# Kernel optimization log

Measured on AMD Instinct MI355X. Metric: run time of the kernel, lower is better.

The kernel has to match this reference:

```python
import jax, jax.numpy as jnp
import numpy as np
from jax import lax

T, B = 256, 64
VOCAB, EMB, HID, NLAB = 100000, 300, 256, 20
PAD_WORD = 0


def setup_inputs() -> dict:
    key = jax.random.key(0)
    ks = jax.random.split(key, 16)
    sentences = jax.random.randint(ks[0], (T, B), 0, VOCAB)
    sentences = sentences.at[0].set(jnp.maximum(sentences[0], 1))  # mask[0] must be all on (torchcrf)
    labels = jax.random.randint(ks[1], (T, B), 0, NLAB)
    s = 0.05
    emb = jax.random.normal(ks[2], (VOCAB, EMB), jnp.float32) * s
    Wih_f = jax.random.normal(ks[3], (4 * HID, EMB), jnp.float32) * s
    Whh_f = jax.random.normal(ks[4], (4 * HID, HID), jnp.float32) * s
    b_f = jax.random.normal(ks[5], (4 * HID,), jnp.float32) * s
    Wih_b = jax.random.normal(ks[6], (4 * HID, EMB), jnp.float32) * s
    Whh_b = jax.random.normal(ks[7], (4 * HID, HID), jnp.float32) * s
    b_b = jax.random.normal(ks[8], (4 * HID,), jnp.float32) * s
    W_top = jax.random.normal(ks[9], (NLAB, 2 * HID), jnp.float32) * s
    b_top = jax.random.normal(ks[10], (NLAB,), jnp.float32) * s
    start_t = jax.random.normal(ks[11], (NLAB,), jnp.float32) * 0.1
    end_t = jax.random.normal(ks[12], (NLAB,), jnp.float32) * 0.1
    trans = jax.random.normal(ks[13], (NLAB, NLAB), jnp.float32) * 0.1
    return dict(emb=emb, Wih_f=Wih_f, Whh_f=Whh_f, b_f=b_f, Wih_b=Wih_b,
                Whh_b=Whh_b, b_b=b_b, W_top=W_top, b_top=b_top,
                start_t=start_t, end_t=end_t, trans=trans,
                sentences=sentences, labels=labels)


def _lstm_dir(x, W_ih, W_hh, b, reverse):
    # x: (T, B, E) -> hs: (T, B, H); torch gate order i,f,g,o
    H = W_hh.shape[1]
    x_proj = jnp.einsum('tbe,ge->tbg', x, W_ih) + b  # precompute input projection

    def step(carry, xp):
        h, c = carry
        gates = xp + h @ W_hh.T
        i, f, g, o = jnp.split(gates, 4, axis=-1)
        c = jax.nn.sigmoid(f) * c + jax.nn.sigmoid(i) * jnp.tanh(g)
        h = jax.nn.sigmoid(o) * jnp.tanh(c)
        return (h, c), h

    init = (jnp.zeros((x.shape[1], H), x.dtype), jnp.zeros((x.shape[1], H), x.dtype))
    _, hs = lax.scan(step, init, x_proj, reverse=reverse)
    return hs


def _crf_nll(emissions, tags, mask, start_t, end_t, trans):
    # emissions: (T,B,L), tags: (T,B), mask: (T,B) bool. torchcrf math, reduction='sum'.
    Tn, Bn, L = emissions.shape
    maskf = mask.astype(emissions.dtype)
    barange = jnp.arange(Bn)
    # numerator
    score = start_t[tags[0]] + emissions[0, barange, tags[0]]
    trans_sc = trans[tags[:-1], tags[1:]]  # (T-1, B)
    emit_sc = jnp.take_along_axis(emissions[1:], tags[1:, :, None], axis=2)[..., 0]
    score = score + ((trans_sc + emit_sc) * maskf[1:]).sum(0)
    seq_ends = mask.astype(jnp.int32).sum(0) - 1  # (B,)
    last_tags = jnp.take_along_axis(tags, seq_ends[None, :], axis=0)[0]
    score = score + end_t[last_tags]
    # partition (log-sum-exp forward recurrence)
    alpha0 = start_t[None, :] + emissions[0]  # (B, L)

    def step(alpha, inp):
        emis_t, m_t = inp
        nxt = jax.nn.logsumexp(alpha[:, :, None] + trans[None] + emis_t[:, None, :], axis=1)
        return jnp.where(m_t[:, None], nxt, alpha), None

    alpha, _ = lax.scan(step, alpha0, (emissions[1:], mask[1:]))
    denom = jax.nn.logsumexp(alpha + end_t[None, :], axis=1)
    llh = (score - denom).sum()
    return -llh


def reference(emb, Wih_f, Whh_f, b_f, Wih_b, Whh_b, b_b, W_top, b_top,
              start_t, end_t, trans, sentences, labels):
    x = emb[sentences]  # (T, B, E)
    h_f = _lstm_dir(x, Wih_f, Whh_f, b_f, reverse=False)
    h_b = _lstm_dir(x, Wih_b, Whh_b, b_b, reverse=True)
    rnn_out = jnp.concatenate([h_f, h_b], axis=-1)  # (T, B, 2H)
    emissions = jnp.einsum('tbh,lh->tbl', rnn_out, W_top) + b_top
    mask = sentences != PAD_WORD
    return _crf_nll(emissions, labels, mask, start_t, end_t, trans)
```

## Files before the change

### kernel.cpp

```cpp
#include <hip/hip_runtime.h>
#include <hip/hip_bf16.h>

#define T_    256
#define B_    64
#define EMB_  300
#define HID_  256
#define G_    1024
#define L_    20
#define M_    (T_*B_)

#define NCL   32
#define CLB   8
#define BPC   4
#define UPB   32

typedef float f32x4 __attribute__((ext_vector_type(4)));
typedef unsigned long long u64;

__global__ __launch_bounds__(256) void k_xproj(
    const float* __restrict__ emb,
    const float* __restrict__ Wih_f, const float* __restrict__ b_f,
    const float* __restrict__ Wih_b, const float* __restrict__ b_b,
    const int*   __restrict__ sent,
    float* __restrict__ xp)
{
    __shared__ float As[16][68];
    __shared__ float Bs[16][68];
    __shared__ int   words[64];

    const int tid = threadIdx.x;
    const int n0  = blockIdx.x * 64;
    const int m0  = blockIdx.y * 64;
    const int dir = n0 >> 10;
    const int g0  = n0 & 1023;
    const float* __restrict__ Wih  = dir ? Wih_b : Wih_f;
    const float* __restrict__ bias = dir ? b_b   : b_f;

    if (tid < 64) words[tid] = sent[m0 + tid];
    __syncthreads();

    const int r = tid >> 2;
    const int q = tid & 3;
    const float* aptr = emb + (size_t)words[r] * EMB_ + q * 4;
    const float* bptr = Wih + (size_t)(g0 + r) * EMB_ + q * 4;

    const int tx = tid & 15;
    const int ty = tid >> 4;
    float acc[4][4] = {};

    for (int k0 = 0; k0 < 304; k0 += 16) {
        const int k = k0 + q * 4;
        float4 av = make_float4(0.f, 0.f, 0.f, 0.f);
        float4 bv = make_float4(0.f, 0.f, 0.f, 0.f);
        if (k < 300) {
            av = *(const float4*)(aptr + k0);
            bv = *(const float4*)(bptr + k0);
        }
        As[q*4+0][r] = av.x; As[q*4+1][r] = av.y; As[q*4+2][r] = av.z; As[q*4+3][r] = av.w;
        Bs[q*4+0][r] = bv.x; Bs[q*4+1][r] = bv.y; Bs[q*4+2][r] = bv.z; Bs[q*4+3][r] = bv.w;
        __syncthreads();
        #pragma unroll
        for (int kk = 0; kk < 16; ++kk) {
            const float4 a = *(const float4*)&As[kk][ty * 4];
            const float4 b = *(const float4*)&Bs[kk][tx * 4];
            acc[0][0] += a.x*b.x; acc[0][1] += a.x*b.y; acc[0][2] += a.x*b.z; acc[0][3] += a.x*b.w;
            acc[1][0] += a.y*b.x; acc[1][1] += a.y*b.y; acc[1][2] += a.y*b.z; acc[1][3] += a.y*b.w;
            acc[2][0] += a.z*b.x; acc[2][1] += a.z*b.y; acc[2][2] += a.z*b.z; acc[2][3] += a.z*b.w;
            acc[3][0] += a.w*b.x; acc[3][1] += a.w*b.y; acc[3][2] += a.w*b.z; acc[3][3] += a.w*b.w;
        }
        __syncthreads();
    }

    float* out = xp + (size_t)dir * M_ * G_;
    const int g = g0 + tx * 4;
    const float4 bs4 = *(const float4*)(bias + g);
    #pragma unroll
    for (int im = 0; im < 4; ++im) {
        const int m = m0 + ty * 4 + im;
        float4 rv;
        rv.x = acc[im][0] + bs4.x;
        rv.y = acc[im][1] + bs4.y;
        rv.z = acc[im][2] + bs4.z;
        rv.w = acc[im][3] + bs4.w;
        *(float4*)(out + (size_t)m * G_ + g) = rv;
    }
}

__global__ __launch_bounds__(256, 1) void k_lstm_scan(
    const float* __restrict__ Whh_f, const float* __restrict__ Whh_b,
    const float* __restrict__ xp, float* __restrict__ hbuf,
    u64* __restrict__ xch)
{
    const int rank = blockIdx.x & 7;
    const int cl   = blockIdx.x >> 3;
    const int dir  = cl >> 4;
    const int bg   = cl & 15;
    const int b0   = bg * BPC;
    const int u0   = rank * UPB;
    const int tid  = threadIdx.x;
    const int lane = tid & 63;
    const int g    = tid >> 6;
    const int r32  = lane & 31;
    const int kh   = lane >> 5;

    const float* __restrict__ Whh = dir ? Whh_b : Whh_f;
    const float* __restrict__ xpd = xp + (size_t)dir * M_ * G_;
    float* __restrict__ hdir = hbuf + (size_t)dir * M_ * HID_;
    u64* __restrict__ xc = xch + ((size_t)dir * B_ + b0) * HID_;

    __shared__ float hs[BPC][264];
    __shared__ float Cg[4][UPB][BPC+1];
    __shared__ float cs[BPC][UPB + 1];

    for (int i = tid; i < BPC * 264; i += 256) ((float*)hs)[i] = 0.f;
    if (tid < BPC * (UPB + 1)) ((float*)cs)[tid] = 0.f;

    f32x4 wv[32];
    {
        const f32x4* wrow = (const f32x4*)(Whh + (size_t)(g * HID_ + u0 + r32) * HID_ + kh * 128);
        #pragma unroll
        for (int i = 0; i < 32; ++i) wv[i] = wrow[i];
    }
    __syncthreads();

    const int eu = tid & 31;
    const int eb = tid >> 5;

    int pb[4], pk[4];
    #pragma unroll
    for (int i = 0; i < 4; ++i) {
        const int idx = i * 256 + tid;
        pb[i] = idx >> 8; pk[i] = idx & 255;
    }

    for (int t = 0; t < T_; ++t) {
        const int t_eff = dir ? (T_ - 1 - t) : t;

        #pragma unroll
        for (int i = 0; i < 32; ++i) asm volatile("" : "+v"(wv[i]));

        float x0 = 0.f, x1 = 0.f, x2 = 0.f, x3 = 0.f;
        if (tid < 128) {
            const float* xrow = xpd + ((size_t)t_eff * B_ + (b0 + eb)) * G_ + (u0 + eu);
            x0 = xrow[0]; x1 = xrow[HID_]; x2 = xrow[2 * HID_]; x3 = xrow[3 * HID_];
        }

        if (t > 0) {
            const unsigned want = (unsigned)t;
            u64 v[4];
            #pragma unroll
            for (int i = 0; i < 4; ++i)
                v[i] = __hip_atomic_load(&xc[(size_t)pb[i] * HID_ + pk[i]],
                                         __ATOMIC_RELAXED, __HIP_MEMORY_SCOPE_AGENT);
            while ((unsigned)(v[0] >> 32) != want || (unsigned)(v[1] >> 32) != want ||
                   (unsigned)(v[2] >> 32) != want || (unsigned)(v[3] >> 32) != want) {
                #pragma unroll
                for (int i = 0; i < 4; ++i)
                    if ((unsigned)(v[i] >> 32) != want)
                        v[i] = __hip_atomic_load(&xc[(size_t)pb[i] * HID_ + pk[i]],
                                                 __ATOMIC_RELAXED, __HIP_MEMORY_SCOPE_AGENT);
            }
            #pragma unroll
            for (int i = 0; i < 4; ++i)
                hs[pb[i]][(pk[i] >> 7) * 132 + (pk[i] & 127)] =
                    __uint_as_float((unsigned)v[i]);
        }
        __syncthreads();

        #pragma unroll
        for (int b = 0; b < BPC; ++b) {
            const f32x4* hv = (const f32x4*)&hs[b][kh * 132];
            float acc = 0.f;
            #pragma unroll
            for (int i = 0; i < 32; ++i) {
                const f32x4 w4 = wv[i];
                const f32x4 h4 = hv[i];
                acc += w4.x * h4.x + w4.y * h4.y + w4.z * h4.z + w4.w * h4.w;
            }
            acc += __shfl_xor(acc, 32);
            if (kh == 0) Cg[g][r32][b] = acc;
        }
        __syncthreads();

        if (tid < 128) {
            const float gi = Cg[0][eu][eb] + x0;
            const float gf = Cg[1][eu][eb] + x1;
            const float gg = Cg[2][eu][eb] + x2;
            const float go = Cg[3][eu][eb] + x3;
            const float i_ = 1.f / (1.f + __expf(-gi));
            const float f_ = 1.f / (1.f + __expf(-gf));
            const float g_ = tanhf(gg);
            const float o_ = 1.f / (1.f + __expf(-go));
            const float cn = f_ * cs[eb][eu] + i_ * g_;
            const float hn = o_ * tanhf(cn);
            cs[eb][eu] = cn;
            if (t + 1 < T_) {
                const u64 pkv = ((u64)(unsigned)(t + 1) << 32) | __float_as_uint(hn);
                __hip_atomic_store(&xc[(size_t)eb * HID_ + (u0 + eu)], pkv,
                                   __ATOMIC_RELAXED, __HIP_MEMORY_SCOPE_AGENT);
            }
            hdir[((size_t)t_eff * B_ + (b0 + eb)) * HID_ + (u0 + eu)] = hn;
        }
    }
}

__global__ __launch_bounds__(256) void k_emis(
    const float* __restrict__ Wt, const float* __restrict__ bt,
    const float* __restrict__ hbuf, float* __restrict__ em)
{
    const int gid = blockIdx.x * 256 + threadIdx.x;
    if (gid >= M_ * L_) return;
    const int m = gid / L_;
    const int l = gid - m * L_;
    const float4* hf  = (const float4*)(hbuf + (size_t)m * HID_);
    const float4* hbk = (const float4*)(hbuf + (size_t)M_ * HID_ + (size_t)m * HID_);
    const float4* w0  = (const float4*)(Wt + (size_t)l * 2 * HID_);
    const float4* w1  = w0 + HID_ / 4;
    float acc = bt[l];
    #pragma unroll 4
    for (int k = 0; k < HID_ / 4; ++k) {
        float4 h = hf[k],  w = w0[k];
        acc += h.x*w.x + h.y*w.y + h.z*w.z + h.w*w.w;
        h = hbk[k]; w = w1[k];
        acc += h.x*w.x + h.y*w.y + h.z*w.z + h.w*w.w;
    }
    em[gid] = acc;
}

__global__ __launch_bounds__(64) void k_crf(
    const float* __restrict__ start_t, const float* __restrict__ end_t,
    const float* __restrict__ trans,
    const int* __restrict__ sent, const int* __restrict__ labels,
    const float* __restrict__ em, float* __restrict__ res)
{
    const int b = blockIdx.x;
    const int tid = threadIdx.x;
    __shared__ float tr[L_ * L_];
    __shared__ float alpha[2][L_];
    __shared__ float red[64];
    __shared__ int   redi[64];
    __shared__ float sdenom;

    for (int i = tid; i < L_ * L_; i += 64) tr[i] = trans[i];
    if (tid < L_) alpha[0][tid] = start_t[tid] + em[b * L_ + tid];
    __syncthreads();

    float pre_em = (tid < L_) ? em[(B_ + b) * L_ + tid] : 0.f;
    int   pre_m  = sent[B_ + b];

    int p = 0;
    for (int t = 1; t < T_; ++t) {
        const float emt = pre_em;
        const int   mt  = pre_m;
        if (t + 1 < T_) {
            if (tid < L_) pre_em = em[((t + 1) * B_ + b) * L_ + tid];
            pre_m = sent[(t + 1) * B_ + b];
        }
        float val = 0.f;
        if (tid < L_) {
            if (mt != 0) {
                float mx = -1e30f;
                #pragma unroll
                for (int i = 0; i < L_; ++i) mx = fmaxf(mx, alpha[p][i] + tr[i * L_ + tid]);
                float s = 0.f;
                #pragma unroll
                for (int i = 0; i < L_; ++i) s += __expf(alpha[p][i] + tr[i * L_ + tid] - mx);
                val = mx + __logf(s) + emt;
            } else {
                val = alpha[p][tid];
            }
        }
        if (tid < L_) alpha[1 - p][tid] = val;
        __syncthreads();
        p ^= 1;
    }

    if (tid == 0) {
        float mx = -1e30f;
        for (int j = 0; j < L_; ++j) mx = fmaxf(mx, alpha[p][j] + end_t[j]);
        float s = 0.f;
        for (int j = 0; j < L_; ++j) s += __expf(alpha[p][j] + end_t[j] - mx);
        sdenom = mx + __logf(s);
    }

    float loc = 0.f;
    int   cnt = 0;
    for (int t = tid; t < T_; t += 64) {
        const int masked = (sent[t * B_ + b] != 0);
        cnt += masked;
        if (t >= 1 && masked) {
            const int tp = labels[(t - 1) * B_ + b];
            const int tc = labels[t * B_ + b];
            loc += tr[tp * L_ + tc] + em[(t * B_ + b) * L_ + tc];
        }
    }
    red[tid] = loc; redi[tid] = cnt;
    __syncthreads();
    if (tid == 0) {
        float s = 0.f; int c = 0;
        for (int i = 0; i < 64; ++i) { s += red[i]; c += redi[i]; }
        const int tag0 = labels[b];
        const int seq_end = c - 1;
        const int last = labels[seq_end * B_ + b];
        const float score = start_t[tag0] + em[b * L_ + tag0] + s + end_t[last];
        res[b] = score - sdenom;
    }
}

__global__ __launch_bounds__(64) void k_final(const float* __restrict__ res,
                                              float* __restrict__ out)
{
    __shared__ float red[64];
    red[threadIdx.x] = res[threadIdx.x];
    __syncthreads();
    if (threadIdx.x == 0) {
        float s = 0.f;
        for (int i = 0; i < 64; ++i) s += red[i];
        out[0] = -s;
    }
}

extern "C" void kernel_launch(void* const* d_in, const int* in_sizes, int n_in,
                              void* d_out, int out_size, void* d_ws, size_t ws_size,
                              hipStream_t stream)
{
    const float* emb     = (const float*)d_in[0];
    const float* Wih_f   = (const float*)d_in[1];
    const float* Whh_f   = (const float*)d_in[2];
    const float* b_f     = (const float*)d_in[3];
    const float* Wih_b   = (const float*)d_in[4];
    const float* Whh_b   = (const float*)d_in[5];
    const float* b_b     = (const float*)d_in[6];
    const float* W_top   = (const float*)d_in[7];
    const float* b_top   = (const float*)d_in[8];
    const float* start_t = (const float*)d_in[9];
    const float* end_t   = (const float*)d_in[10];
    const float* trans   = (const float*)d_in[11];
    const int*   sent    = (const int*)d_in[12];
    const int*   labels  = (const int*)d_in[13];
    float* out = (float*)d_out;

    float* wsf  = (float*)d_ws;
    float* xp   = wsf;
    float* hbuf = xp   + (size_t)2 * M_ * G_;
    float* em   = hbuf + (size_t)2 * M_ * HID_;
    float* res  = em   + (size_t)M_ * L_;
    u64*   xch  = (u64*)(res + 64);

    k_xproj<<<dim3(2048 / 64, M_ / 64), 256, 0, stream>>>(
        emb, Wih_f, b_f, Wih_b, b_b, sent, xp);

    {
        void* args[] = { (void*)&Whh_f, (void*)&Whh_b, (void*)&xp, (void*)&hbuf, (void*)&xch };
        hipLaunchCooperativeKernel((const void*)k_lstm_scan, dim3(256), dim3(256),
                                   args, 0, stream);
    }

    k_emis<<<(M_ * L_ + 255) / 256, 256, 0, stream>>>(W_top, b_top, hbuf, em);

    k_crf<<<B_, 64, 0, stream>>>(start_t, end_t, trans, sent, labels, em, res);

    k_final<<<1, 64, 0, stream>>>(res, out);
}
```

Before: 1.870 ms.

## Remap LSTM scan lanes so gate reduction uses shuffles, drop second barrier

Reassigns thread roles in the recurrent LSTM kernel so each wavefront's lanes hold all four gates and K-halves of a unit. Cross-gate transpose is done with lane shuffles instead of a shared-memory Cg buffer. This removes one __syncthreads per timestep. The h buffer is double-buffered so the next step's writes don't race with readers, and the cell state lives in registers. The risk is extra shuffle/select instructions and half of lanes idle during activation.

```diff
diff --git a/kernel.cpp b/kernel.cpp
--- a/kernel.cpp
+++ b/kernel.cpp
@@ -99,39 +99,32 @@
     const int u0   = rank * UPB;
     const int tid  = threadIdx.x;
     const int lane = tid & 63;
-    const int g    = tid >> 6;
-    const int r32  = lane & 31;
-    const int kh   = lane >> 5;
+    const int w    = tid >> 6;
+    const int kh   = lane & 1;
+    const int gb0  = (lane >> 1) & 1;
+    const int gb1  = (lane >> 2) & 1;
+    const int g    = (lane >> 1) & 3;
+    const int u_loc = (w << 3) | (lane >> 3);
 
     const float* __restrict__ Whh = dir ? Whh_b : Whh_f;
     const float* __restrict__ xpd = xp + (size_t)dir * M_ * G_;
     float* __restrict__ hdir = hbuf + (size_t)dir * M_ * HID_;
     u64* __restrict__ xc = xch + ((size_t)dir * B_ + b0) * HID_;
 
-    __shared__ float hs[BPC][264];
-    __shared__ float Cg[4][UPB][BPC+1];
-    __shared__ float cs[BPC][UPB + 1];
-
-    for (int i = tid; i < BPC * 264; i += 256) ((float*)hs)[i] = 0.f;
-    if (tid < BPC * (UPB + 1)) ((float*)cs)[tid] = 0.f;
+    __shared__ float hs[2][BPC][264];
+
+    for (int i = tid; i < BPC * 264; i += 256) ((float*)hs[0])[i] = 0.f;
 
     f32x4 wv[32];
     {
-        const f32x4* wrow = (const f32x4*)(Whh + (size_t)(g * HID_ + u0 + r32) * HID_ + kh * 128);
+        const f32x4* wrow = (const f32x4*)(Whh + (size_t)(g * HID_ + u0 + u_loc) * HID_ + kh * 128);
         #pragma unroll
         for (int i = 0; i < 32; ++i) wv[i] = wrow[i];
     }
     __syncthreads();
 
-    const int eu = tid & 31;
-    const int eb = tid >> 5;
-
-    int pb[4], pk[4];
-    #pragma unroll
-    for (int i = 0; i < 4; ++i) {
-        const int idx = i * 256 + tid;
-        pb[i] = idx >> 8; pk[i] = idx & 255;
-    }
+    float c_reg = 0.f;
+    const int act = (kh == 0);
 
     for (int t = 0; t < T_; ++t) {
         const int t_eff = dir ? (T_ - 1 - t) : t;
@@ -140,8 +133,8 @@
         for (int i = 0; i < 32; ++i) asm volatile("" : "+v"(wv[i]));
 
         float x0 = 0.f, x1 = 0.f, x2 = 0.f, x3 = 0.f;
-        if (tid < 128) {
-            const float* xrow = xpd + ((size_t)t_eff * B_ + (b0 + eb)) * G_ + (u0 + eu);
+        if (act) {
+            const float* xrow = xpd + ((size_t)t_eff * B_ + (b0 + g)) * G_ + (u0 + u_loc);
             x0 = xrow[0]; x1 = xrow[HID_]; x2 = xrow[2 * HID_]; x3 = xrow[3 * HID_];
         }
 
@@ -150,26 +143,28 @@
             u64 v[4];
             #pragma unroll
             for (int i = 0; i < 4; ++i)
-                v[i] = __hip_atomic_load(&xc[(size_t)pb[i] * HID_ + pk[i]],
+                v[i] = __hip_atomic_load(&xc[(size_t)i * HID_ + tid],
                                          __ATOMIC_RELAXED, __HIP_MEMORY_SCOPE_AGENT);
             while ((unsigned)(v[0] >> 32) != want || (unsigned)(v[1] >> 32) != want ||
                    (unsigned)(v[2] >> 32) != want || (unsigned)(v[3] >> 32) != want) {
                 #pragma unroll
                 for (int i = 0; i < 4; ++i)
                     if ((unsigned)(v[i] >> 32) != want)
-                        v[i] = __hip_atomic_load(&xc[(size_t)pb[i] * HID_ + pk[i]],
+                        v[i] = __hip_atomic_load(&xc[(size_t)i * HID_ + tid],
                                                  __ATOMIC_RELAXED, __HIP_MEMORY_SCOPE_AGENT);
             }
+            float* hw = (float*)hs[t & 1];
             #pragma unroll
             for (int i = 0; i < 4; ++i)
-                hs[pb[i]][(pk[i] >> 7) * 132 + (pk[i] & 127)] =
+                hw[i * 264 + ((tid >> 7) * 132) + (tid & 127)] =
                     __uint_as_float((unsigned)v[i]);
         }
         __syncthreads();
 
+        float a[4];
         #pragma unroll
         for (int b = 0; b < BPC; ++b) {
-            const f32x4* hv = (const f32x4*)&hs[b][kh * 132];
+            const f32x4* hv = (const f32x4*)((const float*)hs[t & 1] + b * 264 + kh * 132);
             float acc = 0.f;
             #pragma unroll
             for (int i = 0; i < 32; ++i) {
@@ -177,29 +172,45 @@
                 const f32x4 h4 = hv[i];
                 acc += w4.x * h4.x + w4.y * h4.y + w4.z * h4.z + w4.w * h4.w;
             }
-            acc += __shfl_xor(acc, 32);
-            if (kh == 0) Cg[g][r32][b] = acc;
-        }
-        __syncthreads();
-
-        if (tid < 128) {
-            const float gi = Cg[0][eu][eb] + x0;
-            const float gf = Cg[1][eu][eb] + x1;
-            const float gg = Cg[2][eu][eb] + x2;
-            const float go = Cg[3][eu][eb] + x3;
+            acc += __shfl_xor(acc, 1);
+            a[b] = acc;
+        }
+
+        const float s01 = gb0 ? a[0] : a[1];
+        const float r01 = __shfl_xor(s01, 2);
+        const float n0 = gb0 ? r01 : a[0];
+        const float n1 = gb0 ? a[1] : r01;
+        const float s23 = gb0 ? a[2] : a[3];
+        const float r23 = __shfl_xor(s23, 2);
+        const float n2 = gb0 ? r23 : a[2];
+        const float n3 = gb0 ? a[3] : r23;
+        const float s02 = gb1 ? n0 : n2;
+        const float r02 = __shfl_xor(s02, 4);
+        const float p0 = gb1 ? r02 : n0;
+        const float p2 = gb1 ? n2 : r02;
+        const float s13 = gb1 ? n1 : n3;
+        const float r13 = __shfl_xor(s13, 4);
+        const float p1 = gb1 ? r13 : n1;
+        const float p3 = gb1 ? n3 : r13;
+
+        if (act) {
+            const float gi = p0 + x0;
+            const float gf = p1 + x1;
+            const float gg = p2 + x2;
+            const float go = p3 + x3;
             const float i_ = 1.f / (1.f + __expf(-gi));
             const float f_ = 1.f / (1.f + __expf(-gf));
             const float g_ = tanhf(gg);
             const float o_ = 1.f / (1.f + __expf(-go));
-            const float cn = f_ * cs[eb][eu] + i_ * g_;
+            const float cn = f_ * c_reg + i_ * g_;
             const float hn = o_ * tanhf(cn);
-            cs[eb][eu] = cn;
+            c_reg = cn;
             if (t + 1 < T_) {
                 const u64 pkv = ((u64)(unsigned)(t + 1) << 32) | __float_as_uint(hn);
-                __hip_atomic_store(&xc[(size_t)eb * HID_ + (u0 + eu)], pkv,
+                __hip_atomic_store(&xc[(size_t)g * HID_ + (u0 + u_loc)], pkv,
                                    __ATOMIC_RELAXED, __HIP_MEMORY_SCOPE_AGENT);
             }
-            hdir[((size_t)t_eff * B_ + (b0 + eb)) * HID_ + (u0 + eu)] = hn;
+            hdir[((size_t)t_eff * B_ + (b0 + g)) * HID_ + (u0 + u_loc)] = hn;
         }
     }
 }
```

Result: faster. 1.799 ms (-3.8%).
